# Optimization experiments

Measured on AMD Instinct MI355X. Metric: run time of the kernel, lower is better.

Reference implementation:

```python
import jax, jax.numpy as jnp
import numpy as np

D_IN = 1024
D_OUT = 1024
SEQ = 4096


def setup_inputs() -> dict:
    key = jax.random.key(0)
    kx, kq, kk, kv = jax.random.split(key, 4)
    s = 1.0 / np.sqrt(D_IN)
    return {
        "x": jax.random.normal(kx, (SEQ, D_IN), dtype=jnp.float32),
        # nn.Linear weights: shape [d_out, d_in], applied as x @ W.T
        "W_q": jax.random.uniform(kq, (D_OUT, D_IN), dtype=jnp.float32, minval=-s, maxval=s),
        "W_k": jax.random.uniform(kk, (D_OUT, D_IN), dtype=jnp.float32, minval=-s, maxval=s),
        "W_v": jax.random.uniform(kv, (D_OUT, D_IN), dtype=jnp.float32, minval=-s, maxval=s),
    }


def reference(x, W_q, W_k, W_v):
    # QKV projections (no bias)
    q = x @ W_q.T  # [N, d_out]
    k = x @ W_k.T
    v = x @ W_v.T
    d_k = k.shape[-1]
    scores = (q @ k.T) / jnp.sqrt(jnp.asarray(d_k, x.dtype))  # [N, N]
    attn = jax.nn.softmax(scores, axis=1)
    n = attn.shape[0]
    mask = jnp.tril(jnp.ones((n, n), dtype=attn.dtype))
    causal = attn * mask
    causal = causal / jnp.sum(causal, axis=1, keepdims=True)
    return causal @ v  # [N, d_out]
```

## Files before the change

### kernel.cpp

```cpp
#include <hip/hip_runtime.h>
#include <hip/hip_bf16.h>
#include <stdint.h>

#define SEQ 4096
#define DIM 1024

typedef __attribute__((ext_vector_type(8))) __bf16 bf16x8;
typedef __attribute__((ext_vector_type(4))) float f32x4;
typedef __attribute__((ext_vector_type(8))) unsigned short u16x8;

__device__ __forceinline__ unsigned short f2bf(float f) {
  unsigned int u = __float_as_uint(f);
  u = (u + 0x7FFFu + ((u >> 16) & 1u)) >> 16;
  return (unsigned short)u;
}

__device__ __forceinline__ int swz(int o) { return o ^ (((o >> 7) & 7) << 4); }

template <int N> __device__ __forceinline__ void wait_vm() {
  if constexpr (N == 0) asm volatile("s_waitcnt vmcnt(0)" ::: "memory");
  else if constexpr (N == 6) asm volatile("s_waitcnt vmcnt(6)" ::: "memory");
  else if constexpr (N == 8) asm volatile("s_waitcnt vmcnt(8)" ::: "memory");
}

__global__ void __launch_bounds__(256) cvt_kernel(const float* __restrict__ src,
                                                  unsigned short* __restrict__ dst) {
  size_t i = (size_t)(blockIdx.x * 256 + threadIdx.x) * 8;
  float4 a = *reinterpret_cast<const float4*>(src + i);
  float4 b = *reinterpret_cast<const float4*>(src + i + 4);
  u16x8 o;
  o[0] = f2bf(a.x); o[1] = f2bf(a.y); o[2] = f2bf(a.z); o[3] = f2bf(a.w);
  o[4] = f2bf(b.x); o[5] = f2bf(b.y); o[6] = f2bf(b.z); o[7] = f2bf(b.w);
  *reinterpret_cast<u16x8*>(dst + i) = o;
}

__global__ void __launch_bounds__(256) cvt3_kernel(const float* __restrict__ wq,
                                                   const float* __restrict__ wk,
                                                   const float* __restrict__ wv,
                                                   unsigned short* __restrict__ wqk,
                                                   unsigned short* __restrict__ wvb) {
  const int z = blockIdx.y;
  const float* src = (z == 0) ? wq : (z == 1) ? wk : wv;
  unsigned short* dst = (z == 2) ? wvb : wqk + (size_t)z * DIM * DIM;
  size_t i = (size_t)(blockIdx.x * 256 + threadIdx.x) * 8;
  float4 a = *reinterpret_cast<const float4*>(src + i);
  float4 b = *reinterpret_cast<const float4*>(src + i + 4);
  u16x8 o;
  o[0] = f2bf(a.x); o[1] = f2bf(a.y); o[2] = f2bf(a.z); o[3] = f2bf(a.w);
  o[4] = f2bf(b.x); o[5] = f2bf(b.y); o[6] = f2bf(b.z); o[7] = f2bf(b.w);
  *reinterpret_cast<u16x8*>(dst + i) = o;
}

template <int BM, int OUT_BF16, int MODE>
__global__ void __launch_bounds__(256) gemm_nt(const unsigned short* __restrict__ A,
                                               const unsigned short* __restrict__ B,
                                               void* __restrict__ C,
                                               float* __restrict__ P1, float* __restrict__ P2,
                                               float* __restrict__ P3,
                                               int lda, int ldb, int ldc, int K, float scale) {
  constexpr int NLA = BM / 32;
  constexpr int NL = NLA + 4;
  constexpr int FM = BM / 32;

  int tc = blockIdx.x, tr = blockIdx.y;
  if (MODE == 1 && tc > tr) return;
  int kt0 = 0, nt = K >> 6;
  if (MODE == 2) {
    const int s = blockIdx.z;
    const int ltiles = tr + 1;
    kt0 = s * 16;
    if (kt0 >= ltiles) return;
    nt = min(ltiles, kt0 + 16) - kt0;
  }

  __shared__ __align__(16) unsigned short As[2][BM * 64];
  __shared__ __align__(16) unsigned short Bs[2][128 * 64];

  const int tid = threadIdx.x;
  const int lane = tid & 63;
  const int wid = tid >> 6;
  const int wr = wid >> 1, wc = wid & 1;
  const int l15 = lane & 15;
  const int kq = lane >> 4;

  f32x4 acc[FM][4];
  #pragma unroll
  for (int m = 0; m < FM; ++m)
    #pragma unroll
    for (int n = 0; n < 4; ++n)
      acc[m][n] = (f32x4){0.f, 0.f, 0.f, 0.f};

  const unsigned short* Abase = A + (size_t)tr * BM * lda;
  const unsigned short* Bbase = B + (size_t)tc * 128 * ldb;

  auto stage = [&](int buf, int ktabs) {
    const int k0 = ktabs << 6;
    #pragma unroll
    for (int i = 0; i < NLA; ++i) {
      const int o = (i * 256 + tid) * 16;
      const int os = swz(o);
      const unsigned short* g = Abase + (size_t)(o >> 7) * lda + k0 + ((os >> 4) & 7) * 8;
      __builtin_amdgcn_global_load_lds(
          (const __attribute__((address_space(1))) unsigned int*)g,
          (__attribute__((address_space(3))) unsigned int*)((char*)&As[buf][0] + o), 16, 0, 0);
    }
    #pragma unroll
    for (int i = 0; i < 4; ++i) {
      const int o = (i * 256 + tid) * 16;
      const int os = swz(o);
      const unsigned short* g = Bbase + (size_t)(o >> 7) * ldb + k0 + ((os >> 4) & 7) * 8;
      __builtin_amdgcn_global_load_lds(
          (const __attribute__((address_space(1))) unsigned int*)g,
          (__attribute__((address_space(3))) unsigned int*)((char*)&Bs[buf][0] + o), 16, 0, 0);
    }
  };

  stage(0, kt0);
  int cur = 0;
  for (int kt = 0; kt < nt; ++kt) {
    if (kt + 1 < nt) {
      stage(cur ^ 1, kt0 + kt + 1);
      wait_vm<NL>();
    } else {
      wait_vm<0>();
    }
    __builtin_amdgcn_s_barrier();

    bf16x8 af[FM][2], bv[4][2];
    #pragma unroll
    for (int m = 0; m < FM; ++m)
      #pragma unroll
      for (int ks = 0; ks < 2; ++ks) {
        const int row = wr * (BM / 2) + m * 16 + l15;
        const int o = swz(row * 128 + kq * 16 + ks * 64);
        af[m][ks] = *reinterpret_cast<const bf16x8*>((const char*)&As[cur][0] + o);
      }
    #pragma unroll
    for (int n = 0; n < 4; ++n)
      #pragma unroll
      for (int ks = 0; ks < 2; ++ks) {
        const int row = wc * 64 + n * 16 + l15;
        const int o = swz(row * 128 + kq * 16 + ks * 64);
        bv[n][ks] = *reinterpret_cast<const bf16x8*>((const char*)&Bs[cur][0] + o);
      }
    #pragma unroll
    for (int m = 0; m < FM; ++m)
      #pragma unroll
      for (int n = 0; n < 4; ++n) {
        acc[m][n] = __builtin_amdgcn_mfma_f32_16x16x32_bf16(af[m][0], bv[n][0], acc[m][n], 0, 0, 0);
        acc[m][n] = __builtin_amdgcn_mfma_f32_16x16x32_bf16(af[m][1], bv[n][1], acc[m][n], 0, 0, 0);
      }
    __builtin_amdgcn_s_barrier();
    cur ^= 1;
  }

  float* fdst = (float*)C;
  int rowoff = 0;
  if (MODE == 2) {
    const int s = blockIdx.z;
    if (s == 1) { fdst = P1; rowoff = 1024; }
    else if (s == 2) { fdst = P2; rowoff = 2048; }
    else if (s == 3) { fdst = P3; rowoff = 3072; }
  }
  const int rbase = tr * BM + wr * (BM / 2) + kq * 4;
  const int cbase = tc * 128 + wc * 64 + l15;
  #pragma unroll
  for (int m = 0; m < FM; ++m)
    #pragma unroll
    for (int n = 0; n < 4; ++n)
      #pragma unroll
      for (int i = 0; i < 4; ++i) {
        const int row = rbase + m * 16 + i;
        const int col = cbase + n * 16;
        float v = acc[m][n][i] * scale;
        if (OUT_BF16)
          ((unsigned short*)C)[(size_t)row * ldc + col] = f2bf(v);
        else
          fdst[(size_t)(row - rowoff) * ldc + col] = v;
      }
}

__global__ void __launch_bounds__(256) reduce_kernel(float* __restrict__ out,
                                                     const float* __restrict__ p1,
                                                     const float* __restrict__ p2,
                                                     const float* __restrict__ p3) {
  const int b = blockIdx.x;
  const size_t e = ((size_t)b * 1024) + threadIdx.x * 4;
  f32x4 acc = *reinterpret_cast<f32x4*>(out + (size_t)1024 * 1024 + e);
  const f32x4 a1 = *reinterpret_cast<const f32x4*>(p1 + e);
  acc += a1;
  if (b >= 1024) acc += *reinterpret_cast<const f32x4*>(p2 + e - (size_t)1024 * 1024);
  if (b >= 2048) acc += *reinterpret_cast<const f32x4*>(p3 + e - (size_t)2048 * 1024);
  *reinterpret_cast<f32x4*>(out + (size_t)1024 * 1024 + e) = acc;
}

__global__ void __launch_bounds__(256) softmax_causal(unsigned short* __restrict__ S) {
  const int row = blockIdx.x;
  const int limit = ((row >> 6) + 1) << 6;
  unsigned short* Srow = S + (size_t)row * SEQ;
  const int tid = threadIdx.x;
  const int lane = tid & 63, wid = tid >> 6;

  float vals[16];
  bool act[2];
  #pragma unroll
  for (int i = 0; i < 2; ++i) {
    const int j0 = (tid + i * 256) * 8;
    act[i] = j0 < limit;
    if (act[i]) {
      const uint4 w = *reinterpret_cast<const uint4*>(Srow + j0);
      const unsigned int wb[4] = {w.x, w.y, w.z, w.w};
      #pragma unroll
      for (int e = 0; e < 4; ++e) {
        vals[i * 8 + 2 * e]     = __uint_as_float(wb[e] << 16);
        vals[i * 8 + 2 * e + 1] = __uint_as_float(wb[e] & 0xFFFF0000u);
      }
    } else {
      #pragma unroll
      for (int e = 0; e < 8; ++e) vals[i * 8 + e] = -1e30f;
    }
  }

  float m = -1e30f;
  #pragma unroll
  for (int i = 0; i < 2; ++i)
    #pragma unroll
    for (int e = 0; e < 8; ++e) {
      int j = (tid + i * 256) * 8 + e;
      if (j <= row) m = fmaxf(m, vals[i * 8 + e]);
    }
  #pragma unroll
  for (int off = 32; off > 0; off >>= 1) m = fmaxf(m, __shfl_xor(m, off));
  __shared__ float redm[4], reds[4];
  if (lane == 0) redm[wid] = m;
  __syncthreads();
  m = fmaxf(fmaxf(redm[0], redm[1]), fmaxf(redm[2], redm[3]));

  float s = 0.f;
  float ev[16];
  #pragma unroll
  for (int i = 0; i < 2; ++i)
    #pragma unroll
    for (int e = 0; e < 8; ++e) {
      int j = (tid + i * 256) * 8 + e;
      float ex = (j <= row) ? __expf(vals[i * 8 + e] - m) : 0.f;
      ev[i * 8 + e] = ex;
      s += ex;
    }
  #pragma unroll
  for (int off = 32; off > 0; off >>= 1) s += __shfl_xor(s, off);
  if (lane == 0) reds[wid] = s;
  __syncthreads();
  s = reds[0] + reds[1] + reds[2] + reds[3];
  const float inv = 1.f / s;

  #pragma unroll
  for (int i = 0; i < 2; ++i) {
    if (!act[i]) continue;
    u16x8 o;
    #pragma unroll
    for (int e = 0; e < 8; ++e) o[e] = f2bf(ev[i * 8 + e] * inv);
    *reinterpret_cast<u16x8*>(Srow + (tid + i * 256) * 8) = o;
  }
}

extern "C" void kernel_launch(void* const* d_in, const int* in_sizes, int n_in,
                              void* d_out, int out_size, void* d_ws, size_t ws_size,
                              hipStream_t stream) {
  const float* x  = (const float*)d_in[0];
  const float* Wq = (const float*)d_in[1];
  const float* Wk = (const float*)d_in[2];
  const float* Wv = (const float*)d_in[3];
  float* out = (float*)d_out;

  char* ws = (char*)d_ws;
  const size_t MB = 1u << 20;
  unsigned short* xb   = (unsigned short*)(ws + 0 * MB);
  unsigned short* wqk  = (unsigned short*)(ws + 8 * MB);
  unsigned short* wvb  = (unsigned short*)(ws + 12 * MB);
  unsigned short* qkb  = (unsigned short*)(ws + 14 * MB);
  unsigned short* vt   = (unsigned short*)(ws + 30 * MB);
  unsigned short* S    = (unsigned short*)(ws + 38 * MB);
  float* p1 = (float*)(ws + 0 * MB);
  float* p2 = (float*)(ws + 12 * MB);
  float* p3 = (float*)(ws + 20 * MB);

  cvt_kernel<<<SEQ * DIM / 2048, 256, 0, stream>>>(x, xb);
  cvt3_kernel<<<dim3(DIM * DIM / 2048, 3), 256, 0, stream>>>(Wq, Wk, Wv, wqk, wvb);

  gemm_nt<128, 1, 0><<<dim3(2048 / 128, SEQ / 128), 256, 0, stream>>>(
      xb, wqk, qkb, nullptr, nullptr, nullptr, DIM, DIM, 2048, DIM, 1.0f);
  gemm_nt<128, 1, 0><<<dim3(SEQ / 128, DIM / 128), 256, 0, stream>>>(
      wvb, xb, vt, nullptr, nullptr, nullptr, DIM, DIM, SEQ, DIM, 1.0f);

  gemm_nt<128, 1, 1><<<dim3(SEQ / 128, SEQ / 128), 256, 0, stream>>>(
      qkb, qkb + 1024, S, nullptr, nullptr, nullptr, 2048, 2048, SEQ, DIM, 0.03125f);

  softmax_causal<<<SEQ, 256, 0, stream>>>(S);

  gemm_nt<64, 0, 2><<<dim3(DIM / 128, SEQ / 64, 4), 256, 0, stream>>>(
      S, vt, out, p1, p2, p3, SEQ, SEQ, DIM, SEQ, 1.0f);
  reduce_kernel<<<3072, 256, 0, stream>>>(out, p1, p2, p3);
}
```

Baseline: 145.8 us.

## Add 256x256-tile 8-wave QK^T kernel with interleaved half-tile prefetch

Replaces the 128x128 causal QK^T GEMM with a dedicated 512-thread kernel computing 256x256 output tiles. Each K step splits its global-to-LDS loads into quarter stages interleaved with MFMA quarters, using barriers and s_setprio, to overlap memory with compute and raise operand reuse per tile. The coarser tiles waste more work on the diagonal blocks of the causal triangle, and the launch has fewer blocks, so fewer CUs may be kept busy.

```diff
diff --git a/kernel.cpp b/kernel.cpp
--- a/kernel.cpp
+++ b/kernel.cpp
@@ -19,6 +19,8 @@
 
 template <int N> __device__ __forceinline__ void wait_vm() {
   if constexpr (N == 0) asm volatile("s_waitcnt vmcnt(0)" ::: "memory");
+  else if constexpr (N == 2) asm volatile("s_waitcnt vmcnt(2)" ::: "memory");
+  else if constexpr (N == 4) asm volatile("s_waitcnt vmcnt(4)" ::: "memory");
   else if constexpr (N == 6) asm volatile("s_waitcnt vmcnt(6)" ::: "memory");
   else if constexpr (N == 8) asm volatile("s_waitcnt vmcnt(8)" ::: "memory");
 }
@@ -51,6 +53,142 @@
   *reinterpret_cast<u16x8*>(dst + i) = o;
 }
 
+__global__ void __launch_bounds__(512) qkt256_kernel(const unsigned short* __restrict__ A,
+                                                     const unsigned short* __restrict__ B,
+                                                     unsigned short* __restrict__ C) {
+  const int tc = blockIdx.x, tr = blockIdx.y;
+  if (tc > tr) return;
+  constexpr int NT = DIM / 64;
+  constexpr int LDA = 2 * DIM, LDB = 2 * DIM, LDC = SEQ;
+  constexpr float SCALE = 0.03125f;
+
+  __shared__ __align__(16) unsigned short As[2][256 * 64];
+  __shared__ __align__(16) unsigned short Bs[2][256 * 64];
+
+  const int tid = threadIdx.x;
+  const int lane = tid & 63;
+  const int wid = tid >> 6;
+  const int wr = wid >> 2;
+  const int wc = wid & 3;
+  const int l15 = lane & 15;
+  const int kq = lane >> 4;
+
+  const unsigned short* Abase = A + (size_t)tr * 256 * LDA;
+  const unsigned short* Bbase = B + (size_t)tc * 256 * LDB;
+
+  f32x4 acc[8][4];
+  #pragma unroll
+  for (int m = 0; m < 8; ++m)
+    #pragma unroll
+    for (int n = 0; n < 4; ++n)
+      acc[m][n] = (f32x4){0.f, 0.f, 0.f, 0.f};
+
+  auto stage_half = [&](int buf, int kt, int h) {
+    const int k0 = kt << 6;
+    const bool isB = (h < 2);
+    unsigned short* lb = isB ? &Bs[buf][0] : &As[buf][0];
+    const unsigned short* gb = isB ? Bbase : Abase;
+    #pragma unroll
+    for (int i = 0; i < 2; ++i) {
+      const int ot = ((h & 1) << 14) + ((i * 512 + tid) << 4);
+      const int row = ot >> 7;
+      const int cs = (swz(ot) >> 4) & 7;
+      const unsigned short* g = gb + (size_t)row * LDA + k0 + cs * 8;
+      __builtin_amdgcn_global_load_lds(
+          (const __attribute__((address_space(1))) unsigned int*)g,
+          (__attribute__((address_space(3))) unsigned int*)((char*)lb + ot), 16, 0, 0);
+    }
+  };
+
+  bf16x8 a[4][2], bn0[2][2], bn1[2][2];
+
+  auto read_A = [&](int b, int mi) {
+    #pragma unroll
+    for (int f = 0; f < 4; ++f) {
+      const int row = wr * 128 + mi * 64 + f * 16 + l15;
+      #pragma unroll
+      for (int ks = 0; ks < 2; ++ks)
+        a[f][ks] = *reinterpret_cast<const bf16x8*>(
+            (const char*)&As[b][0] + swz(row * 128 + kq * 16 + ks * 64));
+    }
+  };
+  auto read_B = [&](int b, int n, bf16x8 (*dst)[2]) {
+    #pragma unroll
+    for (int g = 0; g < 2; ++g) {
+      const int row = wc * 64 + n * 32 + g * 16 + l15;
+      #pragma unroll
+      for (int ks = 0; ks < 2; ++ks)
+        dst[g][ks] = *reinterpret_cast<const bf16x8*>(
+            (const char*)&Bs[b][0] + swz(row * 128 + kq * 16 + ks * 64));
+    }
+  };
+  auto mma_q = [&](int mi, int n, bf16x8 (*bb)[2]) {
+    #pragma unroll
+    for (int f = 0; f < 4; ++f)
+      #pragma unroll
+      for (int g = 0; g < 2; ++g) {
+        acc[mi * 4 + f][n * 2 + g] =
+            __builtin_amdgcn_mfma_f32_16x16x32_bf16(a[f][0], bb[g][0], acc[mi * 4 + f][n * 2 + g], 0, 0, 0);
+        acc[mi * 4 + f][n * 2 + g] =
+            __builtin_amdgcn_mfma_f32_16x16x32_bf16(a[f][1], bb[g][1], acc[mi * 4 + f][n * 2 + g], 0, 0, 0);
+      }
+  };
+
+  stage_half(0, 0, 0); stage_half(0, 0, 1); stage_half(0, 0, 2); stage_half(0, 0, 3);
+  stage_half(1, 1, 0); stage_half(1, 1, 1);
+  wait_vm<4>();
+  __builtin_amdgcn_s_barrier();
+
+  #pragma unroll 1
+  for (int kt = 0; kt < NT; ++kt) {
+    const int b = kt & 1;
+    const bool pf1 = (kt + 1 < NT);
+    const bool pf2 = (kt + 2 < NT);
+    read_A(b, 0);
+    read_B(b, 0, bn0);
+    if (pf1) stage_half(b ^ 1, kt + 1, 2);
+    __builtin_amdgcn_s_barrier();
+    __builtin_amdgcn_s_setprio(1);
+    mma_q(0, 0, bn0);
+    __builtin_amdgcn_s_setprio(0);
+    __builtin_amdgcn_s_barrier();
+    read_B(b, 1, bn1);
+    if (pf1) stage_half(b ^ 1, kt + 1, 3);
+    __builtin_amdgcn_s_barrier();
+    __builtin_amdgcn_s_setprio(1);
+    mma_q(0, 1, bn1);
+    __builtin_amdgcn_s_setprio(0);
+    __builtin_amdgcn_s_barrier();
+    read_A(b, 1);
+    if (pf2) stage_half(b, kt + 2, 0);
+    __builtin_amdgcn_s_barrier();
+    __builtin_amdgcn_s_setprio(1);
+    mma_q(1, 1, bn1);
+    __builtin_amdgcn_s_setprio(0);
+    __builtin_amdgcn_s_barrier();
+    if (pf2) stage_half(b, kt + 2, 1);
+    if (pf1) {
+      if (pf2) wait_vm<4>();
+      else wait_vm<0>();
+    }
+    __builtin_amdgcn_s_barrier();
+    __builtin_amdgcn_s_setprio(1);
+    mma_q(1, 0, bn0);
+    __builtin_amdgcn_s_setprio(0);
+    __builtin_amdgcn_s_barrier();
+  }
+
+  const int rb = tr * 256 + wr * 128 + kq * 4;
+  const int cb = tc * 256 + wc * 64 + l15;
+  #pragma unroll
+  for (int am = 0; am < 8; ++am)
+    #pragma unroll
+    for (int an = 0; an < 4; ++an)
+      #pragma unroll
+      for (int i = 0; i < 4; ++i)
+        C[(size_t)(rb + am * 16 + i) * LDC + cb + an * 16] = f2bf(acc[am][an][i] * SCALE);
+}
+
 template <int BM, int OUT_BF16, int MODE>
 __global__ void __launch_bounds__(256) gemm_nt(const unsigned short* __restrict__ A,
                                                const unsigned short* __restrict__ B,
@@ -63,7 +201,6 @@
   constexpr int FM = BM / 32;
 
   int tc = blockIdx.x, tr = blockIdx.y;
-  if (MODE == 1 && tc > tr) return;
   int kt0 = 0, nt = K >> 6;
   if (MODE == 2) {
     const int s = blockIdx.z;
@@ -187,8 +324,7 @@
   const int b = blockIdx.x;
   const size_t e = ((size_t)b * 1024) + threadIdx.x * 4;
   f32x4 acc = *reinterpret_cast<f32x4*>(out + (size_t)1024 * 1024 + e);
-  const f32x4 a1 = *reinterpret_cast<const f32x4*>(p1 + e);
-  acc += a1;
+  acc += *reinterpret_cast<const f32x4*>(p1 + e);
   if (b >= 1024) acc += *reinterpret_cast<const f32x4*>(p2 + e - (size_t)1024 * 1024);
   if (b >= 2048) acc += *reinterpret_cast<const f32x4*>(p3 + e - (size_t)2048 * 1024);
   *reinterpret_cast<f32x4*>(out + (size_t)1024 * 1024 + e) = acc;
@@ -293,8 +429,7 @@
   gemm_nt<128, 1, 0><<<dim3(SEQ / 128, DIM / 128), 256, 0, stream>>>(
       wvb, xb, vt, nullptr, nullptr, nullptr, DIM, DIM, SEQ, DIM, 1.0f);
 
-  gemm_nt<128, 1, 1><<<dim3(SEQ / 128, SEQ / 128), 256, 0, stream>>>(
-      qkb, qkb + 1024, S, nullptr, nullptr, nullptr, 2048, 2048, SEQ, DIM, 0.03125f);
+  qkt256_kernel<<<dim3(SEQ / 256, SEQ / 256), 512, 0, stream>>>(qkb, qkb + 1024, S);
 
   softmax_causal<<<SEQ, 256, 0, stream>>>(S);
 
```

After: 141.8 us. 2.7% less time.
